# Optimization experiments

Measured on AMD Instinct MI355X. Metric: run time of the kernel, lower is better.

Reference implementation:

```python
import jax, jax.numpy as jnp
import numpy as np

DEPTH = 256
HEADS = 8
K = 128          # kernel_size == attended axis length (height)
DH = DEPTH // HEADS  # 32
EPS = 1e-5


def _bn(x, gamma, beta, axes):
    # training-mode batch norm (biased variance), per-channel on axis 1
    mean = jnp.mean(x, axis=axes, keepdims=True)
    var = jnp.var(x, axis=axes, keepdims=True)
    shape = [1] * x.ndim
    shape[1] = x.shape[1]
    g = gamma.reshape(shape)
    b = beta.reshape(shape)
    return (x - mean) * jax.lax.rsqrt(var + EPS) * g + b


def setup_inputs() -> dict:
    key = jax.random.key(0)
    ks = jax.random.split(key, 3)
    x = jax.random.normal(ks[0], (2, DEPTH, K, K), dtype=jnp.float32)
    w_kqv = jax.random.normal(ks[1], (2 * DEPTH, DEPTH), dtype=jnp.float32) * 0.05
    rel_encoding = jax.random.normal(ks[2], (2 * DH, 2 * K - 1), dtype=jnp.float32)
    return {
        "x": x,
        "w_kqv": w_kqv,
        "kqv_gamma": jnp.ones((2 * DEPTH,), jnp.float32),
        "kqv_beta": jnp.zeros((2 * DEPTH,), jnp.float32),
        "logits_gamma": jnp.ones((3 * HEADS,), jnp.float32),
        "logits_beta": jnp.zeros((3 * HEADS,), jnp.float32),
        "rel_encoding": rel_encoding,
    }


def reference(x, w_kqv, kqv_gamma, kqv_beta, logits_gamma, logits_beta, rel_encoding):
    B, C, H, W = x.shape  # height_dim=True path
    # (B,C,H,W) -> (B,W,C,H) -> (B*W, C, H)
    xf = jnp.transpose(x, (0, 3, 1, 2)).reshape(B * W, C, H)
    # 1x1 conv == channel matmul
    kqv = jnp.einsum('oc,bch->boh', w_kqv, xf)  # (BW, 2*depth, H)
    kqv = _bn(kqv, kqv_gamma, kqv_beta, axes=(0, 2))
    kqv = kqv.reshape(B * W, HEADS, 2 * DH, H)
    k = kqv[:, :, : DH // 2]            # (BW, h, dh/2, H)
    q = kqv[:, :, DH // 2: DH]          # (BW, h, dh/2, H)
    v = kqv[:, :, DH:]                  # (BW, h, dh,   H)

    # relative position gather: (2*dh, 2K-1) -> (2*dh, K, K)
    idx = (jnp.arange(K)[None, :] - jnp.arange(K)[:, None] + K - 1).reshape(-1)
    rel = rel_encoding[:, idx].reshape(2 * DH, K, K)
    q_enc = rel[: DH // 2]
    k_enc = rel[DH // 2: DH]
    v_enc = rel[DH:]

    qk = jnp.einsum('bhdx,bhdy->bhxy', q, k)
    qr = jnp.einsum('bhdx,dxy->bhxy', q, q_enc)
    kr = jnp.swapaxes(jnp.einsum('bhdx,dxy->bhxy', k, k_enc), 2, 3)
    logits = jnp.concatenate([qk, qr, kr], axis=1)  # (BW, 3*h, K, K)
    logits = _bn(logits, logits_gamma, logits_beta, axes=(0, 2, 3))
    logits = logits.reshape(B * W, 3, HEADS, H, H).sum(axis=1)
    weights = jax.nn.softmax(logits, axis=3)  # (BW, h, K, K)

    attn = jnp.einsum('bhxy,bhdy->bhdx', weights, v)         # (BW, h, dh, H)
    attn_enc = jnp.einsum('bhxy,dxy->bhdx', weights, v_enc)  # (BW, h, dh, H)
    out = (attn + attn_enc).reshape(B, W, DEPTH, H)  # cat+reshape+sum(dim=-2) == add
    out = jnp.transpose(out, (0, 2, 3, 1))  # (B, depth, H, W)
    return out
```

## Files before the change

kernel.cpp:

```cpp
#include <hip/hip_runtime.h>
#include <hip/hip_bf16.h>

#define H 128
#define NB 256
#define OC 512
#define CIN 256
#define NN 16384
#define EPS 1e-5f

#define EQG_OFF 524288
#define EKG_OFF 589824
#define EVG_OFF 655360

typedef __attribute__((ext_vector_type(4))) float f32x4;
typedef __attribute__((ext_vector_type(8))) short bf16x8;
typedef unsigned short u16x8 __attribute__((ext_vector_type(8)));
typedef unsigned int u32x4 __attribute__((ext_vector_type(4)));

__device__ __forceinline__ float bf2f(unsigned short u){
    return __uint_as_float(((unsigned int)u) << 16);
}
__device__ __forceinline__ unsigned short f2bf(float f){
    unsigned int r;
    asm("v_cvt_pk_bf16_f32 %0, %1, %2" : "=v"(r) : "v"(f), "v"(f));
    return (unsigned short)r;
}
__device__ __forceinline__ unsigned int f2bf2(float a, float b){
    unsigned int r;
    asm("v_cvt_pk_bf16_f32 %0, %1, %2" : "=v"(r) : "v"(a), "v"(b));
    return r;
}
__device__ __forceinline__ float ldin(const void* p, size_t i, bool f32){
    return f32 ? ((const float*)p)[i] : bf2f(((const unsigned short*)p)[i]);
}
__device__ __forceinline__ short ld_bf16(const void* p, size_t i, bool f32){
    if (f32) return (short)f2bf(((const float*)p)[i]);
    return ((const short*)p)[i];
}
__device__ __forceinline__ bool probe_f32(const void* gamma_ones){
    return *(const unsigned int*)gamma_ones == 0x3F800000u;
}

template<bool F32>
__device__ __forceinline__ void gemm_body(const void* __restrict__ w,
                                          const void* __restrict__ x,
                                          unsigned short* __restrict__ c1,
                                          short (*As)[128][40], short (*Bs)[128][40],
                                          int m0, int n0, int b0)
{
    const int t  = threadIdx.x;
    const int lane = t & 63, wv = t >> 6;
    const int wm = wv & 1, wn = wv >> 1;
    const int lm = lane & 15, quad = lane >> 4;
    const size_t xb = (size_t)b0 * CIN * NN;
    const int am = t >> 1, ak = (t & 1) * 16;
    const int bn = t & 127, bk = (t >> 7) * 16;

    float4 pa[4]; float pb[16];
    u16x8 qa[2]; unsigned short qb[16];

    auto load_tile = [&](int k0){
        if constexpr (F32){
            const float* wp = (const float*)w + (size_t)(m0+am)*CIN + k0 + ak;
            #pragma unroll
            for (int q=0;q<4;q++) pa[q] = *(const float4*)(wp + 4*q);
            const float* xp = (const float*)x + xb + (size_t)(k0+bk)*NN + n0 + bn;
            #pragma unroll
            for (int i=0;i<16;i++) pb[i] = xp[(size_t)i*NN];
        } else {
            const unsigned short* wp = (const unsigned short*)w + (size_t)(m0+am)*CIN + k0 + ak;
            qa[0] = *(const u16x8*)wp; qa[1] = *(const u16x8*)(wp+8);
            const unsigned short* xp = (const unsigned short*)x + xb + (size_t)(k0+bk)*NN + n0 + bn;
            #pragma unroll
            for (int i=0;i<16;i++) qb[i] = xp[(size_t)i*NN];
        }
    };
    auto store_tile = [&](int buf){
        if constexpr (F32){
            u32x4 ua0, ua1;
            ua0[0]=f2bf2(pa[0].x,pa[0].y); ua0[1]=f2bf2(pa[0].z,pa[0].w);
            ua0[2]=f2bf2(pa[1].x,pa[1].y); ua0[3]=f2bf2(pa[1].z,pa[1].w);
            ua1[0]=f2bf2(pa[2].x,pa[2].y); ua1[1]=f2bf2(pa[2].z,pa[2].w);
            ua1[2]=f2bf2(pa[3].x,pa[3].y); ua1[3]=f2bf2(pa[3].z,pa[3].w);
            *(u32x4*)&As[buf][am][ak]   = ua0;
            *(u32x4*)&As[buf][am][ak+8] = ua1;
            u32x4 ub0, ub1;
            #pragma unroll
            for (int i=0;i<4;i++) ub0[i] = f2bf2(pb[2*i], pb[2*i+1]);
            #pragma unroll
            for (int i=0;i<4;i++) ub1[i] = f2bf2(pb[8+2*i], pb[8+2*i+1]);
            *(u32x4*)&Bs[buf][bn][bk]   = ub0;
            *(u32x4*)&Bs[buf][bn][bk+8] = ub1;
        } else {
            *(u16x8*)&As[buf][am][ak]   = qa[0];
            *(u16x8*)&As[buf][am][ak+8] = qa[1];
            *(u16x8*)&Bs[buf][bn][bk]   = *(u16x8*)&qb[0];
            *(u16x8*)&Bs[buf][bn][bk+8] = *(u16x8*)&qb[8];
        }
    };

    f32x4 acc[4][4];
    #pragma unroll
    for (int i=0;i<4;i++)
        #pragma unroll
        for (int j=0;j<4;j++) acc[i][j]=(f32x4){0,0,0,0};

    load_tile(0); store_tile(0); __syncthreads();
    for (int kk=0; kk<8; ++kk){
        const int cur = kk & 1;
        if (kk < 7) load_tile((kk+1)*32);
        bf16x8 af[4], bfB[4];
        #pragma unroll
        for (int i=0;i<4;i++) af[i]  = *(const bf16x8*)&As[cur][wm*64 + i*16 + lm][quad*8];
        #pragma unroll
        for (int j=0;j<4;j++) bfB[j] = *(const bf16x8*)&Bs[cur][wn*64 + j*16 + lm][quad*8];
        #pragma unroll
        for (int i=0;i<4;i++)
            #pragma unroll
            for (int j=0;j<4;j++)
                acc[i][j] = __builtin_amdgcn_mfma_f32_16x16x32_bf16(af[i], bfB[j], acc[i][j], 0,0,0);
        if (kk < 7) store_tile(cur ^ 1);
        __syncthreads();
    }
    #pragma unroll
    for (int i=0;i<4;i++){
        #pragma unroll
        for (int j=0;j<4;j++){
            int n = n0 + wn*64 + j*16 + lm;
            #pragma unroll
            for (int r=0;r<4;r++){
                int m = m0 + wm*64 + i*16 + quad*4 + r;
                c1[((size_t)b0*OC + m)*NN + n] = f2bf(acc[i][j][r]);
            }
        }
    }
}

__global__ __launch_bounds__(256) void k_gemm(const void* __restrict__ w,
                                              const void* __restrict__ x,
                                              unsigned short* __restrict__ c1,
                                              const void* __restrict__ probe)
{
    __shared__ short As[2][128][40];
    __shared__ short Bs[2][128][40];
    const int bid = blockIdx.x;
    const int swz = (bid & 7)*128 + (bid >> 3);
    const int m0 = (swz & 3)*128;
    const int n0 = ((swz >> 2) & 127)*128;
    const int b0 = swz >> 9;
    if (probe_f32(probe)) gemm_body<true >(w, x, c1, As, Bs, m0, n0, b0);
    else                  gemm_body<false>(w, x, c1, As, Bs, m0, n0, b0);
}

__global__ __launch_bounds__(256) void k_bn_transpose(const unsigned short* __restrict__ c1,
        unsigned short* __restrict__ kqvt,
        const void* __restrict__ gamma, const void* __restrict__ beta)
{
    __shared__ short T[128][130];
    __shared__ float red[8];
    __shared__ float sc_sh[2];
    const bool f32 = probe_f32(gamma);
    const int o  = blockIdx.x;
    const int b0 = blockIdx.y;
    const int t = threadIdx.x;
    const int lane = t & 63, wv = t >> 6;
    const u16x8* r08 = (const u16x8*)(c1 + (size_t)o*NN);
    const u16x8* r18 = (const u16x8*)(c1 + ((size_t)OC + o)*NN);
    float sp[4] = {0,0,0,0}, qp[4] = {0,0,0,0};
    #pragma unroll
    for (int i=0;i<8;i++){
        u16x8 a = r08[t + i*256];
        u16x8 b = r18[t + i*256];
        #pragma unroll
        for (int e=0;e<8;e++){
            float va = bf2f(a[e]); sp[e&3] += va; qp[e&3] = fmaf(va,va,qp[e&3]);
            float vb = bf2f(b[e]); sp[e&3] += vb; qp[e&3] = fmaf(vb,vb,qp[e&3]);
        }
    }
    float s = (sp[0]+sp[1])+(sp[2]+sp[3]);
    float ss = (qp[0]+qp[1])+(qp[2]+qp[3]);
    #pragma unroll
    for (int off=1; off<64; off<<=1){ s += __shfl_xor(s,off); ss += __shfl_xor(ss,off); }
    if (lane==0){ red[wv*2] = s; red[wv*2+1] = ss; }
    __syncthreads();
    if (t==0){
        float st=0.f, sq=0.f;
        for (int i=0;i<4;i++){ st += red[i*2]; sq += red[i*2+1]; }
        float mean = st * (1.f/32768.f);
        float var  = sq * (1.f/32768.f) - mean*mean;
        float scale = ldin(gamma, o, f32) * rsqrtf(var + EPS);
        sc_sh[0] = scale;
        sc_sh[1] = ldin(beta, o, f32) - mean*scale;
    }
    __syncthreads();
    const float scale = sc_sh[0], shift = sc_sh[1];
    const u16x8* r8 = b0 ? r18 : r08;
    #pragma unroll
    for (int i=0;i<8;i++){
        int vi = t + i*256;
        u16x8 a = r8[vi];
        int n0_ = vi*8;
        int h = n0_ >> 7, ww = n0_ & 127;
        #pragma unroll
        for (int e=0;e<8;e++) T[ww+e][h] = (short)a[e];
    }
    __syncthreads();
    #pragma unroll
    for (int i=0;i<8;i++){
        int vi = t + i*256;
        int ww = vi >> 4, h8 = (vi & 15)*8;
        u16x8 tv = *(const u16x8*)&T[ww][h8];
        unsigned short outv[8];
        #pragma unroll
        for (int e=0;e<8;e++)
            outv[e] = f2bf(fmaf(bf2f((unsigned short)tv[e]), scale, shift));
        *(u16x8*)&kqvt[(((size_t)(b0*128 + ww))*OC + o)*H + h8] = *(u16x8*)outv;
    }
}

__global__ __launch_bounds__(256) void k_encpre(const void* __restrict__ relenc,
        float* __restrict__ ws, const void* __restrict__ probe)
{
    __shared__ float E[16][256];
    const bool f32 = probe_f32(probe);
    const int grp = blockIdx.x;
    const int t = threadIdx.x;
    if (grp == 2){
        unsigned short* ev = (unsigned short*)ws + EVG_OFF;
        for (int i = t; i < 32*264; i += 256){
            int d = i / 264, j = i - d*264;
            ev[i] = (j < 255) ? (unsigned short)ld_bf16(relenc, (size_t)(32+d)*255 + j, f32) : 0;
        }
        return;
    }
    for (int i = t; i < 16*255; i += 256){
        int d = i / 255, j = i - d*255;
        E[d][j] = bf2f((unsigned short)ld_bf16(relenc, (size_t)(grp*16 + d)*255 + j, f32));
    }
    __syncthreads();
    float* Rout = ws + 256  + grp*2048;
    float* Cout = ws + 8192 + grp*32768;
    {
        const int d = t >> 4, e = t & 15;
        const float* Ed = E[d]; const float* Ee = E[e];
        float c = 0.f;
        for (int j = 0; j < 128; ++j) c = fmaf(Ed[j], Ee[j], c);
        float* Cp = Cout + (d*16+e)*128;
        Cp[127] = c;
        for (int xx = 126; xx >= 0; --xx){
            c += Ed[254-xx]*Ee[254-xx] - Ed[126-xx]*Ee[126-xx];
            Cp[xx] = c;
        }
    }
    if (t < 16){
        const float* Ed = E[t];
        float r = 0.f;
        for (int j = 0; j < 128; ++j) r += Ed[j];
        float* Rp = Rout + t*128;
        Rp[127] = r;
        for (int xx = 126; xx >= 0; --xx){
            r += Ed[254-xx] - Ed[126-xx];
            Rp[xx] = r;
        }
    }
}

__global__ __launch_bounds__(256) void k_stats2(const unsigned short* __restrict__ kqvt,
        const float* __restrict__ ws, float* __restrict__ stats)
{
    __shared__ short QK[2][16][128];
    __shared__ float wr[4][6];
    const int b = blockIdx.x >> 3, head = blockIdx.x & 7;
    const int t = threadIdx.x;
    const int lane = t & 63, wv = t >> 6;
    const int lm = lane & 15, quad = lane >> 4;
    const unsigned short* base = kqvt + ((size_t)b*OC + head*64)*H;
    for (int i = t; i < 512; i += 256){
        int arr = i >> 8, d = (i >> 4) & 15, c = i & 15;
        *(u16x8*)&QK[arr][d][c*8] = *(const u16x8*)&base[(size_t)(arr*16 + d)*H + c*8];
    }
    __syncthreads();

    float s_qk = 0.f, q_qk = 0.f;
    if (wv == 0){
        f32x4 gq  = (f32x4){0,0,0,0}, gk  = (f32x4){0,0,0,0};
        f32x4 gq1 = (f32x4){0,0,0,0}, gk1 = (f32x4){0,0,0,0};
        bf16x8 ones;
        #pragma unroll
        for (int i=0;i<8;i++) ones[i] = (short)0x3F80;
        #pragma unroll
        for (int xt=0; xt<4; ++xt){
            bf16x8 fq = *(const bf16x8*)&QK[1][lm][xt*32 + quad*8];
            bf16x8 fk = *(const bf16x8*)&QK[0][lm][xt*32 + quad*8];
            gq  = __builtin_amdgcn_mfma_f32_16x16x32_bf16(fq, fq,   gq,  0,0,0);
            gk  = __builtin_amdgcn_mfma_f32_16x16x32_bf16(fk, fk,   gk,  0,0,0);
            gq1 = __builtin_amdgcn_mfma_f32_16x16x32_bf16(fq, ones, gq1, 0,0,0);
            gk1 = __builtin_amdgcn_mfma_f32_16x16x32_bf16(fk, ones, gk1, 0,0,0);
        }
        #pragma unroll
        for (int r=0;r<4;r++) q_qk += gq[r]*gk[r];
        if (lm == 0){
            #pragma unroll
            for (int r=0;r<4;r++) s_qk += gq1[r]*gk1[r];
        }
    }

    const int half = t >> 7;
    const int x = t & 127;
    float col[16];
    #pragma unroll
    for (int d=0; d<16; ++d) col[d] = bf2f((unsigned short)QK[1-half][d][x]);
    const float* Rp = ws + 256  + half*2048;
    const float* Cp = ws + 8192 + half*32768;
    float sr = 0.f;
    #pragma unroll
    for (int d=0; d<16; ++d) sr = fmaf(col[d], Rp[d*128 + x], sr);
    float q2p[4] = {0,0,0,0};
    #pragma unroll
    for (int d=0; d<16; ++d){
        float qd = col[d];
        q2p[d&3] = fmaf(qd*qd, Cp[(d*17)*128 + x], q2p[d&3]);
        #pragma unroll
        for (int e=d+1; e<16; ++e)
            q2p[e&3] = fmaf(2.f*qd*col[e], Cp[(d*16+e)*128 + x], q2p[e&3]);
    }
    float q2 = (q2p[0]+q2p[1]) + (q2p[2]+q2p[3]);
    float s_qr = half ? 0.f : sr,  q_qr = half ? 0.f : q2;
    float s_kr = half ? sr : 0.f,  q_kr = half ? q2 : 0.f;

    #pragma unroll
    for (int off=1; off<64; off<<=1){
        s_qk += __shfl_xor(s_qk,off); q_qk += __shfl_xor(q_qk,off);
        s_qr += __shfl_xor(s_qr,off); q_qr += __shfl_xor(q_qr,off);
        s_kr += __shfl_xor(s_kr,off); q_kr += __shfl_xor(q_kr,off);
    }
    if (lane==0){ wr[wv][0]=s_qk; wr[wv][1]=s_qr; wr[wv][2]=s_kr;
                  wr[wv][3]=q_qk; wr[wv][4]=q_qr; wr[wv][5]=q_kr; }
    __syncthreads();
    if (t==0){
        float a0=0,a1=0,a2=0,b0_=0,b1=0,b2=0;
        for (int i=0;i<4;i++){ a0+=wr[i][0]; a1+=wr[i][1]; a2+=wr[i][2];
                               b0_+=wr[i][3]; b1+=wr[i][4]; b2+=wr[i][5]; }
        atomicAdd(&stats[head],      a0);
        atomicAdd(&stats[8+head],    a1);
        atomicAdd(&stats[16+head],   a2);
        atomicAdd(&stats[24+head],   b0_);
        atomicAdd(&stats[32+head],   b1);
        atomicAdd(&stats[40+head],   b2);
    }
}

__global__ void k_scales(const float* __restrict__ stats, float* __restrict__ scales,
                         const void* __restrict__ gamma_l, const void* __restrict__ probe)
{
    const bool f32 = probe_f32(probe);
    int t = threadIdx.x;
    if (t < 24){
        const float inv_cnt = 1.f/4194304.f;
        float mean = stats[t]*inv_cnt;
        float var  = stats[24+t]*inv_cnt - mean*mean;
        scales[t] = ldin(gamma_l, t, f32) * rsqrtf(var + EPS);
    }
}

__global__ void k_escale(const void* __restrict__ relenc, const float* __restrict__ scales,
                         unsigned short* __restrict__ etab, const void* __restrict__ probe)
{
    const bool f32 = probe_f32(probe);
    const int head = blockIdx.x;
    const int t = threadIdx.x;
    const float s1 = scales[8+head], s2 = scales[16+head];
    unsigned short* eq = etab + EQG_OFF + head*8192;
    unsigned short* ek = etab + EKG_OFF + head*8192;
    for (int i = t; i < 8192; i += 256){
        int j = i >> 5, c = i & 31;
        unsigned short vq = 0, vk = 0;
        if (c < 16 && j < 255){
            vq = f2bf(s1 * ldin(relenc, (size_t)c*255 + j, f32));
            vk = f2bf(s2 * ldin(relenc, (size_t)(16+c)*255 + j, f32));
        }
        eq[i] = vq; ek[i] = vk;
    }
}

__global__ __launch_bounds__(256) void k_attn(const unsigned short* __restrict__ kqvt,
        const unsigned short* __restrict__ etab,
        const float* __restrict__ scales,
        void* __restrict__ outp,
        const void* __restrict__ probe)
{
    __shared__ short KA[128][24];
    __shared__ short RW[128][130];
    __shared__ alignas(16) short ZED[16];
    const bool f32 = probe_f32(probe);
    const int blk = blockIdx.x;
    const int b = blk >> 3, head = blk & 7;
    const int b0 = b >> 7, w = b & 127;
    const int t = threadIdx.x;
    const int lane = t & 63, wv = t >> 6;
    const int lm = lane & 15, quad = lane >> 4;
    const unsigned short* base = kqvt + ((size_t)b*OC + head*64)*H;
    const float s0 = scales[head];
    const unsigned short* EQg = etab + EQG_OFF + (size_t)head*8192;
    const unsigned short* EKg = etab + EKG_OFF + (size_t)head*8192;
    const unsigned short* EVg = etab + EVG_OFF;

    {
        int dd = t & 15, xg = (t >> 4) * 8;
        u16x8 kv = *(const u16x8*)&base[dd*H + xg];
        #pragma unroll
        for (int e=0;e<8;e++) KA[xg+e][dd] = (short)kv[e];
    }
    bf16x8 aq[2];
    #pragma unroll
    for (int u=0;u<2;u++){
        aq[u] = (bf16x8){0,0,0,0,0,0,0,0};
        if (quad < 2){
            const int x = (2*wv+u)*16 + lm;
            const unsigned short* qp = base + (16+quad*8)*H + x;
            #pragma unroll
            for (int e=0;e<8;e++) aq[u][e] = (short)qp[(size_t)e*H];
        }
    }
    if (t < 16) ZED[t] = 0;
    __syncthreads();

    bf16x8 akk[2];
    #pragma unroll
    for (int u=0;u<2;u++){
        akk[u] = (bf16x8){0,0,0,0,0,0,0,0};
        if (quad < 2) akk[u] = *(const bf16x8*)&KA[(2*wv+u)*16 + lm][quad*8];
    }

    f32x4 qacc[2][8];
    #pragma unroll
    for (int u=0;u<2;u++){
        const int mt = 2*wv + u;
        #pragma unroll
        for (int yt=0; yt<8; ++yt){
            const short* pb = (quad < 2) ? &KA[yt*16 + lm][quad*8] : &ZED[0];
            bf16x8 bk = *(const bf16x8*)pb;
            qacc[u][yt] = __builtin_amdgcn_mfma_f32_16x16x32_bf16(aq[u], bk,
                            (f32x4){0.f,0.f,0.f,0.f}, 0,0,0);
        }
        #pragma unroll
        for (int jj=0; jj<9; ++jj){
            const int jt = 7 - mt + jj;
            bf16x8 bq = *(const bf16x8*)&EQg[(size_t)(jt*16 + lm)*32 + quad*8];
            f32x4 cq = __builtin_amdgcn_mfma_f32_16x16x32_bf16(aq[u], bq,
                         (f32x4){0.f,0.f,0.f,0.f}, 0,0,0);
            int j = jt*16 + lm;
            #pragma unroll
            for (int r=0;r<4;r++){
                int x = mt*16 + quad*4 + r;
                int y = x + j - 127;
                if ((unsigned)y < 128u) RW[x][y] = (short)f2bf(cq[r]);
            }
        }
    }
    __syncthreads();

    #pragma unroll
    for (int u=0;u<2;u++){
        const int mt = 2*wv + u;
        #pragma unroll
        for (int jj=0; jj<9; ++jj){
            const int jt = 7 - mt + jj;
            bf16x8 bkE = *(const bf16x8*)&EKg[(size_t)(jt*16 + lm)*32 + quad*8];
            f32x4 ck = __builtin_amdgcn_mfma_f32_16x16x32_bf16(akk[u], bkE,
                         (f32x4){0.f,0.f,0.f,0.f}, 0,0,0);
            int j = jt*16 + lm;
            #pragma unroll
            for (int r=0;r<4;r++){
                int y = mt*16 + quad*4 + r;
                int x = y + j - 127;
                if ((unsigned)x < 128u){
                    float cur = bf2f((unsigned short)RW[x][y]);
                    RW[x][y] = (short)f2bf(cur + ck[r]);
                }
            }
        }
    }
    __syncthreads();

    #pragma unroll
    for (int u=0;u<2;u++){
        const int mt = 2*wv + u;
        #pragma unroll
        for (int r=0;r<4;r++){
            const int x = mt*16 + quad*4 + r;
            float v[8]; float mx = -1e30f;
            #pragma unroll
            for (int yt=0; yt<8; ++yt){
                v[yt] = fmaf(s0, qacc[u][yt][r], bf2f((unsigned short)RW[x][yt*16 + lm]));
                mx = fmaxf(mx, v[yt]);
            }
            mx = fmaxf(mx, __shfl_xor(mx,1));
            mx = fmaxf(mx, __shfl_xor(mx,2));
            mx = fmaxf(mx, __shfl_xor(mx,4));
            mx = fmaxf(mx, __shfl_xor(mx,8));
            float sum = 0.f;
            #pragma unroll
            for (int yt=0; yt<8; ++yt){ v[yt] = __expf(v[yt]-mx); sum += v[yt]; }
            sum += __shfl_xor(sum,1);
            sum += __shfl_xor(sum,2);
            sum += __shfl_xor(sum,4);
            sum += __shfl_xor(sum,8);
            float inv = 1.f/sum;
            #pragma unroll
            for (int yt=0; yt<8; ++yt)
                RW[x][yt*16 + lm] = (short)f2bf(v[yt]*inv);
        }
    }
    __syncthreads();

    f32x4 o[2][2];
    #pragma unroll
    for (int u=0;u<2;u++){ o[u][0]=(f32x4){0,0,0,0}; o[u][1]=(f32x4){0,0,0,0}; }
    #pragma unroll
    for (int kt=0; kt<4; ++kt){
        bf16x8 bv0 = *(const bf16x8*)&base[(size_t)(32+lm)*H + kt*32 + quad*8];
        bf16x8 bv1 = *(const bf16x8*)&base[(size_t)(48+lm)*H + kt*32 + quad*8];
        #pragma unroll
        for (int u=0;u<2;u++){
            bf16x8 aw = *(const bf16x8*)&RW[(2*wv+u)*16 + lm][kt*32 + quad*8];
            o[u][0] = __builtin_amdgcn_mfma_f32_16x16x32_bf16(aw, bv0, o[u][0], 0,0,0);
            o[u][1] = __builtin_amdgcn_mfma_f32_16x16x32_bf16(aw, bv1, o[u][1], 0,0,0);
        }
    }
    #pragma unroll
    for (int u=0;u<2;u++){
        const int mt = 2*wv + u;
        const int ktlo = (112 - mt*16) >> 5;
        const int xg = mt*16 + lm;
        #pragma unroll
        for (int jj=0; jj<5; ++jj){
            const int kt = ktlo + jj;
            bf16x8 be0 = *(const bf16x8*)&EVg[(size_t)lm*264      + kt*32 + quad*8];
            bf16x8 be1 = *(const bf16x8*)&EVg[(size_t)(16+lm)*264 + kt*32 + quad*8];
            int y0 = xg + kt*32 + quad*8 - 127;
            short g[8];
            #pragma unroll
            for (int jjj=0;jjj<8;jjj++){
                int y = y0 + jjj;
                g[jjj] = ((unsigned)y < 128u) ? RW[xg][y] : (short)0;
            }
            bf16x8 ag = *(bf16x8*)g;
            o[u][0] = __builtin_amdgcn_mfma_f32_16x16x32_bf16(ag, be0, o[u][0], 0,0,0);
            o[u][1] = __builtin_amdgcn_mfma_f32_16x16x32_bf16(ag, be1, o[u][1], 0,0,0);
        }
    }
    #pragma unroll
    for (int u=0;u<2;u++){
        #pragma unroll
        for (int nt=0; nt<2; ++nt){
            int d = nt*16 + lm;
            size_t cb = ((size_t)(b0*256 + head*32 + d))*16384 + (size_t)w;
            #pragma unroll
            for (int r=0;r<4;r++){
                int x = (2*wv+u)*16 + quad*4 + r;
                if (f32) ((float*)outp)[cb + (size_t)x*128] = o[u][nt][r];
                else ((unsigned short*)outp)[cb + (size_t)x*128] = f2bf(o[u][nt][r]);
            }
        }
    }
}

extern "C" void kernel_launch(void* const* d_in, const int* in_sizes, int n_in,
                              void* d_out, int out_size, void* d_ws, size_t ws_size,
                              hipStream_t stream)
{
    (void)in_sizes; (void)n_in; (void)out_size;
    const void* x      = d_in[0];
    const void* w_kqv  = d_in[1];
    const void* kqv_g  = d_in[2];
    const void* kqv_b  = d_in[3];
    const void* log_g  = d_in[4];
    const void* relenc = d_in[6];

    if (ws_size < (size_t)64*1024*1024) return;
    unsigned short* C1   = (unsigned short*)d_ws;
    unsigned short* KQVT = C1 + 16777216;
    float* WS     = (float*)d_ws;
    float* STATS  = WS;
    float* SCALES = WS + 48;
    unsigned short* ETAB = (unsigned short*)d_ws;

    k_gemm<<<1024, 256, 0, stream>>>(w_kqv, x, C1, kqv_g);
    k_bn_transpose<<<dim3(512,2), 256, 0, stream>>>(C1, KQVT, kqv_g, kqv_b);
    hipMemsetAsync(STATS, 0, 48*sizeof(float), stream);
    k_encpre<<<3, 256, 0, stream>>>(relenc, WS, kqv_g);
    k_stats2<<<2048, 256, 0, stream>>>(KQVT, WS, STATS);
    k_scales<<<1, 64, 0, stream>>>(STATS, SCALES, log_g, kqv_g);
    k_escale<<<8, 256, 0, stream>>>(relenc, SCALES, ETAB, kqv_g);
    k_attn<<<2048, 256, 0, stream>>>(KQVT, ETAB, SCALES, d_out, kqv_g);
}
```

Baseline: 346.8 us.

## Fuse kqv batch-norm statistics into GEMM epilogue via partial sums

The GEMM epilogue now reduces each output channel's sum and sum of squares across its tile from fp32 accumulators. It writes per-slice partials into a scratch area that aliases the output buffer. The BN/transpose kernel reads 512 partials per channel instead of re-reading both batches of the bf16 intermediate, which removes a full extra pass over C1. It adds shuffle reductions and small strided stores to the GEMM, and depends on the output buffer being free until the attention kernel overwrites it.

```diff
diff --git a/kernel.cpp b/kernel.cpp
--- a/kernel.cpp
+++ b/kernel.cpp
@@ -45,6 +45,7 @@
 __device__ __forceinline__ void gemm_body(const void* __restrict__ w,
                                           const void* __restrict__ x,
                                           unsigned short* __restrict__ c1,
+                                          float* __restrict__ part,
                                           short (*As)[128][40], short (*Bs)[128][40],
                                           int m0, int n0, int b0)
 {
@@ -134,11 +135,36 @@
             }
         }
     }
+    {
+        const int slice = b0*256 + (n0 >> 7)*2 + wn;
+        #pragma unroll
+        for (int i=0;i<4;i++){
+            #pragma unroll
+            for (int r=0;r<4;r++){
+                float s = 0.f, ss = 0.f;
+                #pragma unroll
+                for (int j=0;j<4;j++){
+                    float v = acc[i][j][r];
+                    s += v; ss = fmaf(v, v, ss);
+                }
+                #pragma unroll
+                for (int off=1; off<16; off<<=1){
+                    s += __shfl_xor(s, off); ss += __shfl_xor(ss, off);
+                }
+                if (lm == 0){
+                    int m = m0 + wm*64 + i*16 + quad*4 + r;
+                    float2* pp = (float2*)part + (size_t)m*512 + slice;
+                    *pp = make_float2(s, ss);
+                }
+            }
+        }
+    }
 }
 
 __global__ __launch_bounds__(256) void k_gemm(const void* __restrict__ w,
                                               const void* __restrict__ x,
                                               unsigned short* __restrict__ c1,
+                                              float* __restrict__ part,
                                               const void* __restrict__ probe)
 {
     __shared__ short As[2][128][40];
@@ -148,13 +174,14 @@
     const int m0 = (swz & 3)*128;
     const int n0 = ((swz >> 2) & 127)*128;
     const int b0 = swz >> 9;
-    if (probe_f32(probe)) gemm_body<true >(w, x, c1, As, Bs, m0, n0, b0);
-    else                  gemm_body<false>(w, x, c1, As, Bs, m0, n0, b0);
+    if (probe_f32(probe)) gemm_body<true >(w, x, c1, part, As, Bs, m0, n0, b0);
+    else                  gemm_body<false>(w, x, c1, part, As, Bs, m0, n0, b0);
 }
 
 __global__ __launch_bounds__(256) void k_bn_transpose(const unsigned short* __restrict__ c1,
         unsigned short* __restrict__ kqvt,
-        const void* __restrict__ gamma, const void* __restrict__ beta)
+        const void* __restrict__ gamma, const void* __restrict__ beta,
+        const float* __restrict__ part)
 {
     __shared__ short T[128][130];
     __shared__ float red[8];
@@ -164,24 +191,13 @@
     const int b0 = blockIdx.y;
     const int t = threadIdx.x;
     const int lane = t & 63, wv = t >> 6;
-    const u16x8* r08 = (const u16x8*)(c1 + (size_t)o*NN);
-    const u16x8* r18 = (const u16x8*)(c1 + ((size_t)OC + o)*NN);
-    float sp[4] = {0,0,0,0}, qp[4] = {0,0,0,0};
-    #pragma unroll
-    for (int i=0;i<8;i++){
-        u16x8 a = r08[t + i*256];
-        u16x8 b = r18[t + i*256];
-        #pragma unroll
-        for (int e=0;e<8;e++){
-            float va = bf2f(a[e]); sp[e&3] += va; qp[e&3] = fmaf(va,va,qp[e&3]);
-            float vb = bf2f(b[e]); sp[e&3] += vb; qp[e&3] = fmaf(vb,vb,qp[e&3]);
-        }
-    }
-    float s = (sp[0]+sp[1])+(sp[2]+sp[3]);
-    float ss = (qp[0]+qp[1])+(qp[2]+qp[3]);
-    #pragma unroll
-    for (int off=1; off<64; off<<=1){ s += __shfl_xor(s,off); ss += __shfl_xor(ss,off); }
-    if (lane==0){ red[wv*2] = s; red[wv*2+1] = ss; }
+    {
+        float4 v = ((const float4*)(part + (size_t)o*1024))[t];
+        float s = v.x + v.z, ss = v.y + v.w;
+        #pragma unroll
+        for (int off=1; off<64; off<<=1){ s += __shfl_xor(s,off); ss += __shfl_xor(ss,off); }
+        if (lane==0){ red[wv*2] = s; red[wv*2+1] = ss; }
+    }
     __syncthreads();
     if (t==0){
         float st=0.f, sq=0.f;
@@ -194,7 +210,7 @@
     }
     __syncthreads();
     const float scale = sc_sh[0], shift = sc_sh[1];
-    const u16x8* r8 = b0 ? r18 : r08;
+    const u16x8* r8 = (const u16x8*)(c1 + ((size_t)(b0*OC) + o)*NN);
     #pragma unroll
     for (int i=0;i<8;i++){
         int vi = t + i*256;
@@ -585,9 +601,10 @@
     float* STATS  = WS;
     float* SCALES = WS + 48;
     unsigned short* ETAB = (unsigned short*)d_ws;
-
-    k_gemm<<<1024, 256, 0, stream>>>(w_kqv, x, C1, kqv_g);
-    k_bn_transpose<<<dim3(512,2), 256, 0, stream>>>(C1, KQVT, kqv_g, kqv_b);
+    float* PART   = (float*)d_out;
+
+    k_gemm<<<1024, 256, 0, stream>>>(w_kqv, x, C1, PART, kqv_g);
+    k_bn_transpose<<<dim3(512,2), 256, 0, stream>>>(C1, KQVT, kqv_g, kqv_b, PART);
     hipMemsetAsync(STATS, 0, 48*sizeof(float), stream);
     k_encpre<<<3, 256, 0, stream>>>(relenc, WS, kqv_g);
     k_stats2<<<2048, 256, 0, stream>>>(KQVT, WS, STATS);
```

Result: no change. 343.4 us (-1.0%).
